# Performance work log

Measured on AMD Instinct MI355X. Metric: run time of the kernel, lower is better.

Reference implementation:

```python
import jax, jax.numpy as jnp
import numpy as np

BETA1, BETA2, BETA3 = 0.9, 0.8, 0.9
DECAY1, INC1 = 0.05, 5.0
DECAY3, INC3 = 0.05, 5.0
LATENCY = 4.0
B_CONST = 0.15
LIF1_MIN, LIF1_MAX = 150.0, 400.0
LIF3_MIN, LIF3_MAX = 50.0, 200.0
A_P, A_M, TAU_P, TAU_M = 0.01, 0.01, 20.0, 20.0  # exponential STDP params (params1/2/3)


def stdp(dt):
    # exponential STDP curve: potentiate when post fires after pre (dt>=0), depress otherwise
    return jnp.where(dt >= 0, A_P * jnp.exp(-dt / TAU_P), -A_M * jnp.exp(dt / TAU_M))


def setup_inputs() -> dict:
    key = jax.random.key(0)
    k1, k2, k3, k4 = jax.random.split(key, 4)
    H, N, C = 8192, 4096, 128
    return {
        "image": jax.random.uniform(k1, (N,), jnp.float32),
        "W1": jax.random.uniform(k2, (H, N), jnp.float32),
        "W2": jax.random.uniform(k3, (N, H), jnp.float32),
        "W3": jax.random.uniform(k4, (C, N), jnp.float32),
        "thr1": 100.0 * jnp.ones((H,), jnp.float32),
        "thr2": 5.0 * jnp.ones((N,), jnp.float32),
        "thr3": 100.0 * jnp.ones((C,), jnp.float32),
        "time": 256,
        "pw": 8,
    }


def reference(image, W1, W2, W3, thr1, thr2, thr3, time, pw):
    N = image.shape[0]
    H = W1.shape[0]
    C = W3.shape[0]
    T = int(time)
    Tf = jnp.float32(T)

    img_t = Tf * image  # input spike times, [N]
    # rate -> pulse encoding: input_spikes[t, i] = 1 for t in [floor(img_t[i]), floor(img_t[i])+pw)
    t_axis = jnp.arange(T, dtype=jnp.float32)[:, None]          # [T,1]
    start = jnp.floor(img_t)[None, :]                            # [1,N]
    input_spikes = ((t_axis >= start) & (t_axis < start + pw)).astype(jnp.float32)  # [T,N]

    def wta(mem, th):
        # winner-take-all (snntorch inhibition=True): only argmax neuron may spike
        j = jnp.argmax(mem)
        fire = (mem[j] > th[j]).astype(mem.dtype)
        return fire * jax.nn.one_hot(j, mem.shape[0], dtype=mem.dtype)

    def step(carry, xs):
        mem1, mem2, mem3, th1, th3, r1, r2, r3, hid_act, out_act = carry
        x, t = xs
        # layer 1: Leaky LIF, inhibition, reset-to-zero
        mem1 = BETA1 * mem1 + jnp.dot(W1, x)
        spk1 = wta(mem1, th1)
        mem1 = mem1 * (1.0 - spk1)
        # layer 2: Leaky LIF, no inhibition, reset-by-subtract
        mem2 = BETA2 * mem2 + jnp.dot(W2, spk1)
        spk2 = (mem2 > thr2).astype(mem2.dtype)
        mem2 = mem2 - spk2 * thr2
        # layer 3 (clustering): Leaky LIF, inhibition, zeroed after any spike
        mem3 = BETA3 * mem3 + jnp.dot(W3, spk2)
        spk3 = wta(mem3, th3)
        mem3 = mem3 - spk3 * th3
        mem3 = jnp.where(jnp.sum(spk3) > 0, 0.0, mem3)
        # first-spike-time recon (recon stays at first nonzero spk*(t+1))
        r1 = jnp.where(r1 != 0, r1, spk1 * (t + 1.0))
        r2 = jnp.where(r2 != 0, r2, spk2 * (t + 1.0))
        r3 = jnp.where(r3 != 0, r3, spk3 * (t + 1.0))
        hid_act = hid_act + spk1
        out_act = out_act + spk2
        # adaptive thresholds: homeostatic decay + spike-triggered increase, clamped
        th1 = jnp.clip(th1 - DECAY1 + INC1 * spk1, LIF1_MIN, LIF1_MAX)
        th3 = jnp.clip(th3 - DECAY3 + INC3 * spk3, LIF3_MIN, LIF3_MAX)
        return (mem1, mem2, mem3, th1, th3, r1, r2, r3, hid_act, out_act), None

    z = jnp.zeros
    carry0 = (z(H), z(N), z(C), thr1, thr3, z(H), z(N), z(C), z(H), z(N))
    (mem1, mem2, mem3, th1, th3, r1, r2, r3, hid_act, out_act), _ = jax.lax.scan(
        step, carry0, (input_spikes, jnp.arange(T, dtype=jnp.float32)))

    # neurons that never spiked get time T
    r1 = jnp.where(r1 == 0, Tf, r1)
    r2 = jnp.where(r2 == 0, Tf, r2)
    r3 = jnp.where(r3 == 0, Tf, r3)

    # STDP weight updates (exponential), same structure as PresentImage
    hid_mask = (hid_act > 0).astype(jnp.float32)
    delta_t1 = (r1[:, None] - img_t[None, :]) * hid_mask[:, None]      # [H,N]
    W1_new = W1 + stdp(delta_t1)
    delta_t2 = r2[:, None] - r1[None, :]                                # [N,H]
    zeta = (Tf - r1) * hid_mask / Tf                                    # [H]
    rho = (r2 - LATENCY - img_t) / Tf + B_CONST                         # [N]
    W2_new = jnp.clip(W2 + stdp(delta_t2) * (rho[:, None] * zeta[None, :]), 0.0, 1.0)
    delta_t3 = r3[:, None] - r2[None, :]                                # [C,N]
    W3_new = W3 + stdp(delta_t3)

    error = (img_t - (r2 - LATENCY)) / Tf
    error_scalar = jnp.sum(jnp.square(error))
    return (error, error_scalar, r1, r2, r3, W1_new, W2_new, W3_new)
```

## Files before the change

kernel.cpp:

```cpp
#include <hip/hip_runtime.h>
#include <cstdint>
#include <cstddef>

#define Hn 8192
#define Nn 4096
#define Cn 128
#define Tt 256
#define CAP 192
#define CHUNK 8
#define RING 16

typedef unsigned long long ull;

__device__ __forceinline__ float th_lazy2(float b, float lo, float hi, int nup){
    if (nup <= 0) return b;
    float a = fminf(fmaxf(__fsub_rn(b, 0.05f), lo), hi);
    if (nup == 1) return a;
    return fmaxf(__fsub_rn(a, __fmul_rn(0.05f, (float)(nup - 1))), lo);
}

__device__ __forceinline__ float clamp01(float v){
    return fminf(fmaxf(v, 0.f), 1.f);
}

template<int CTRL>
__device__ __forceinline__ int dpp_i(int x, int old){
    return __builtin_amdgcn_update_dpp(old, x, CTRL, 0xf, 0xf, false);
}
__device__ __forceinline__ float wave_max_f(float v){
    const int NEG = __float_as_int(-3.4e38f);
#define STEPM(C) { float o = __int_as_float(dpp_i<C>(__float_as_int(v), NEG)); v = fmaxf(v, o); }
    STEPM(0x111) STEPM(0x112) STEPM(0x114) STEPM(0x118) STEPM(0x142) STEPM(0x143)
#undef STEPM
    return __int_as_float(__builtin_amdgcn_readlane(__float_as_int(v), 63));
}
__device__ __forceinline__ int wave_argmax_l(float bv, int bh, float &wv, int &wh){
    float v = wave_max_f(bv);
    ull tie = __ballot(bv == v);
    int tl = __ffsll((long long)tie) - 1;
    int h = __builtin_amdgcn_readlane(bh, tl);
    if (__builtin_expect(__popcll(tie) > 1, 0)){
        ull m = tie & (tie - 1);
        while (m){
            int l2 = __ffsll((long long)m) - 1;
            int h2 = __builtin_amdgcn_readlane(bh, l2);
            if (h2 < h){ h = h2; tl = l2; }
            m &= m - 1;
        }
    }
    wv = v; wh = h; return tl;
}
__device__ __forceinline__ float rl_f(float x, int l){
    return __int_as_float(__builtin_amdgcn_readlane(__float_as_int(x), l));
}

__global__ __launch_bounds__(1024) void k_prep(const float* __restrict__ image,
        int* __restrict__ boff, int* __restrict__ sidx, unsigned* __restrict__ anyv,
        float* __restrict__ imgt, float* __restrict__ eiP, float* __restrict__ eiM){
    __shared__ int s_start[Nn];
    __shared__ int s_c4[4][Tt];
    __shared__ int s_boff[Tt + 1];
    int tid = threadIdx.x;
    for (int i = tid; i < Nn; i += 1024){
        float im = image[i];
        float img = __fmul_rn(256.f, im);
        s_start[i] = (int)floorf(img);
        imgt[i] = img;
        eiP[i] = __expf(img * 0.05f);
        eiM[i] = __expf(-img * 0.05f);
    }
    if (tid < Tt) anyv[tid] = 0u;
    __syncthreads();
    int b = tid & 255, q = tid >> 8;
    {
        int c = 0;
        for (int k = 0; k < 1024; ++k) c += (s_start[q * 1024 + k] == b) ? 1 : 0;
        s_c4[q][b] = c;
    }
    __syncthreads();
    if (tid == 0){
        int acc = 0;
        for (int bb = 0; bb < Tt; ++bb){
            s_boff[bb] = acc;
            acc += s_c4[0][bb] + s_c4[1][bb] + s_c4[2][bb] + s_c4[3][bb];
        }
        s_boff[Tt] = acc;
    }
    __syncthreads();
    if (tid <= Tt) boff[tid] = s_boff[tid];
    int p = s_boff[b];
    if (q > 0) p += s_c4[0][b];
    if (q > 1) p += s_c4[1][b];
    if (q > 2) p += s_c4[2][b];
    for (int k = 0; k < 1024; ++k){
        int i = q * 1024 + k;
        if (s_start[i] == b) sidx[p++] = i;
    }
}

__global__ __launch_bounds__(256) void k_gbuckets(const float* __restrict__ W1,
        const int* __restrict__ boff, const int* __restrict__ sidx,
        float* __restrict__ G_T, float* __restrict__ o_W1){
    __shared__ float rows[2][Nn];
    int tid = threadIdx.x;
    int h0 = blockIdx.x * 2;
    for (int r = 0; r < 2; ++r){
        const float4* src = (const float4*)(W1 + (size_t)(h0 + r) * Nn);
        float4* dst = (float4*)rows[r];
        for (int j = tid; j < Nn / 4; j += 256) dst[j] = src[j];
    }
    __syncthreads();
    int t = tid;
    int b0 = boff[t], b1 = boff[t + 1];
    float s0 = 0.f, s1 = 0.f;
    for (int k = b0; k < b1; ++k){
        int i = sidx[k];
        s0 += rows[0][i]; s1 += rows[1][i];
    }
    G_T[(size_t)(h0 + 0) * Tt + t] = s0;
    G_T[(size_t)(h0 + 1) * Tt + t] = s1;
    for (int r = 0; r < 2; ++r){
        const float4* srw = (const float4*)rows[r];
        float4* dw = (float4*)(o_W1 + (size_t)(h0 + r) * Nn);
        for (int j = tid; j < Nn / 4; j += 256){
            float4 s = srw[j];
            s.x = __fadd_rn(s.x, 0.01f); s.y = __fadd_rn(s.y, 0.01f);
            s.z = __fadd_rn(s.z, 0.01f); s.w = __fadd_rn(s.w, 0.01f);
            dw[j] = s;
        }
    }
}

__global__ __launch_bounds__(256) void k_c1M(const float* __restrict__ G_T,
        float* __restrict__ M, float* __restrict__ r1pre, float* __restrict__ o_r1){
    __shared__ float tile[32][Tt + 1];
    __shared__ float c1s[32][Tt + 1];
    const int tid = threadIdx.x;
    const int h0 = blockIdx.x * 32;
    for (int r = 0; r < 32; ++r) tile[r][tid] = G_T[(size_t)(h0 + r) * Tt + tid];
    __syncthreads();
    {
        int hs = tid & 31, ts = tid >> 5;
        for (int tb = 0; tb < 32; ++tb){
            int t = tb * 8 + ts;
            int lo = (t - 7 < 0) ? 0 : t - 7;
            float s = 0.f;
            for (int u = lo; u <= t; ++u) s += tile[hs][u];
            c1s[hs][t] = s;
        }
    }
    __syncthreads();
    if (tid < 32){
        float m = 0.f;
        for (int t = 0; t < Tt; ++t){
            m = __fadd_rn(__fmul_rn(0.9f, m), c1s[tid][t]);
            M[(size_t)t * Hn + h0 + tid] = m;
        }
        r1pre[h0 + tid] = 0.f;
        o_r1[h0 + tid] = 256.f;
    }
}

__global__ __launch_bounds__(256) void k_sel(const float* __restrict__ M,
        float2* __restrict__ cand2, float* __restrict__ gvcap){
    const int t = blockIdx.x, tid = threadIdx.x;
    __shared__ float s_row[Hn];
    __shared__ unsigned s_hist[256];
    __shared__ unsigned s_suf[256];
    __shared__ unsigned s_pref;
    __shared__ int s_rank;
    __shared__ int s_cnt;
    __shared__ int s_idx[CAP + 64];
    {
        const float4* src = (const float4*)(M + (size_t)t * Hn);
        float4* d4 = (float4*)s_row;
        for (int j = tid; j < Hn / 4; j += 256) d4[j] = src[j];
    }
    if (tid == 0){ s_pref = 0u; s_rank = CAP; s_cnt = 0; }
    __syncthreads();
#pragma unroll
    for (int b = 3; b >= 0; --b){
        s_hist[tid] = 0u;
        __syncthreads();
        unsigned pref = s_pref;
        int r = s_rank;
        for (int k = 0; k < 32; ++k){
            unsigned u = __float_as_uint(s_row[tid + (k << 8)]);
            bool match = (b == 3) ? true : ((u >> ((b + 1) * 8)) == pref);
            if (match) atomicAdd(&s_hist[(u >> (b * 8)) & 255], 1u);
        }
        __syncthreads();
        s_suf[tid] = s_hist[tid];
        __syncthreads();
#pragma unroll
        for (int off = 1; off < 256; off <<= 1){
            unsigned v = (tid + off < 256) ? s_suf[tid + off] : 0u;
            __syncthreads();
            s_suf[tid] += v;
            __syncthreads();
        }
        unsigned above = s_suf[tid] - s_hist[tid];
        if ((int)above < r && r <= (int)s_suf[tid]){
            s_pref = (pref << 8) | (unsigned)tid;
            s_rank = r - (int)above;
        }
        __syncthreads();
    }
    unsigned V = s_pref;
    for (int k = 0; k < 32; ++k){
        int i = tid + (k << 8);
        unsigned u = __float_as_uint(s_row[i]);
        if (u >= V){
            int p = atomicAdd(&s_cnt, 1);
            if (p < CAP + 64) s_idx[p] = i;
        }
    }
    __syncthreads();
    int c = s_cnt;
    bool ovf = (c > CAP);
    if (tid == 0) gvcap[t] = ovf ? 3.4e38f : __uint_as_float(V);
    for (int i = tid; i < CAP; i += 256){
        float2 e;
        if (!ovf && i < c){
            int ix = s_idx[i];
            e = make_float2(s_row[ix], __int_as_float(ix | (1 << 15)));
        } else {
            e = make_float2(-1.f, 0.f);
        }
        cand2[(size_t)t * CAP + i] = e;
    }
}

#define NB_W2 1024
#define NB_W3T 128

union FusedLDS {
    struct {
        float4 mst[Hn];
        float2 ring[RING][CAP];
        float  vcr[RING];
        int j1[Tt];
        unsigned bm[256];
    } w;
    float tl[64][65];
};

__global__ __launch_bounds__(1024, 1) void k_fused(
        const float* __restrict__ M, const float2* __restrict__ cand2,
        const float* __restrict__ gvcap, const float* __restrict__ thr1,
        const float* __restrict__ W2, const float* __restrict__ W3,
        float* __restrict__ o_W2, float* __restrict__ W3T,
        float* __restrict__ r1pre, float* __restrict__ o_r1,
        int* __restrict__ j1s, int* __restrict__ mh, int* __restrict__ nRout){
    __shared__ FusedLDS u;
    const int bid = blockIdx.x;
    const int tid = threadIdx.x;

    if (bid >= 1 && bid < 1 + NB_W2){
        size_t base = (size_t)(bid - 1) * 8192;
        const float4* src = (const float4*)W2;
        float4* dst = (float4*)o_W2;
        for (int i = tid; i < 8192; i += 4096){
            float4 a0 = src[base + i];
            float4 a1 = src[base + i + 1024];
            float4 a2 = src[base + i + 2048];
            float4 a3 = src[base + i + 3072];
            a0.x = clamp01(a0.x); a0.y = clamp01(a0.y); a0.z = clamp01(a0.z); a0.w = clamp01(a0.w);
            a1.x = clamp01(a1.x); a1.y = clamp01(a1.y); a1.z = clamp01(a1.z); a1.w = clamp01(a1.w);
            a2.x = clamp01(a2.x); a2.y = clamp01(a2.y); a2.z = clamp01(a2.z); a2.w = clamp01(a2.w);
            a3.x = clamp01(a3.x); a3.y = clamp01(a3.y); a3.z = clamp01(a3.z); a3.w = clamp01(a3.w);
            dst[base + i]        = a0;
            dst[base + i + 1024] = a1;
            dst[base + i + 2048] = a2;
            dst[base + i + 3072] = a3;
        }
        return;
    }
    if (bid >= 1 + NB_W2){
        int r = bid - 1 - NB_W2;
        int bx = r & 63, by = r >> 6;
        int n0 = bx * 64, c0 = by * 64;
        for (int e = tid; e < 64 * 64; e += 1024){
            int rr = e >> 6, cc = e & 63;
            u.tl[rr][cc] = W3[(size_t)(c0 + rr) * Nn + n0 + cc];
        }
        __syncthreads();
        for (int e = tid; e < 64 * 64; e += 1024){
            int rn = e >> 6, cc = e & 63;
            W3T[(size_t)(n0 + rn) * Cn + c0 + cc] = u.tl[cc][rn];
        }
        return;
    }

    for (int h = tid; h < Hn; h += 1024)
        u.w.mst[h] = make_float4(0.f, -1.f, thr1[h], 0.f);
    for (int e = tid; e < CHUNK * CAP; e += 1024){
        int so = e / CAP, j = e - so * CAP;
        u.w.ring[so][j] = cand2[(size_t)so * CAP + j];
    }
    if (tid < CHUNK) u.w.vcr[tid] = gvcap[tid];
    __syncthreads();

    const int lane = tid & 63;
    const float Lc = -0.15200309344504997f;

    for (int c = 0; c < Tt / CHUNK; ++c){
        if (tid >= 64 && c + 1 < Tt / CHUNK){
            for (int e = tid - 64; e < CHUNK * CAP; e += 960){
                int so = e / CAP, j = e - so * CAP;
                int step = (c + 1) * CHUNK + so;
                u.w.ring[step & (RING - 1)][j] = cand2[(size_t)step * CAP + j];
            }
            if (tid - 64 < CHUNK){
                int step = (c + 1) * CHUNK + (tid - 64);
                u.w.vcr[step & (RING - 1)] = gvcap[step];
            }
        }
        if (tid < 64){
            for (int s = 0; s < CHUNK; ++s){
                const int t = c * CHUNK + s;
                const int slot = t & (RING - 1);
                const float tf = (float)t;
                float2 e0 = u.w.ring[slot][lane];
                float2 e1 = u.w.ring[slot][64 + lane];
                float2 e2 = u.w.ring[slot][128 + lane];
                float vc = u.w.vcr[slot];
                int m0b = __float_as_int(e0.y), m1b = __float_as_int(e1.y), m2b = __float_as_int(e2.y);
                int h0 = m0b & 8191, h1 = m1b & 8191, h2 = m2b & 8191;
                float4 g0 = u.w.mst[h0];
                float4 g1 = u.w.mst[h1];
                float4 g2 = u.w.mst[h2];
                float bm = -3.4e38f; int bhh = 0x7FFFFFFF;
                float braw = 0.f, bts = 0.f, bthb = 0.f;
#define CPROC(ee, mb, hh, gg) { \
                float dd = __fsub_rn(tf, gg.y); \
                float mem = __fsub_rn(ee.x, __fmul_rn(exp2f(__fmul_rn(dd, Lc)), gg.x)); \
                if (!((mb >> 15) & 1)) mem = -3.4e38f; \
                if (mem > bm || (mem == bm && hh < bhh)){ bm = mem; bhh = hh; braw = ee.x; bts = gg.y; bthb = gg.z; } }
                CPROC(e0, m0b, h0, g0) CPROC(e1, m1b, h1, g1) CPROC(e2, m2b, h2, g2)
#undef CPROC
                float wv; int wh;
                int wl = wave_argmax_l(bm, bhh, wv, wh);
                float raw = rl_f(braw, wl), tsv = rl_f(bts, wl), thb = rl_f(bthb, wl);
                int skip = 0;
                if (__builtin_expect(wv < vc, 0)){
                    if (t > 0 && vc < 150.f){
                        skip = 1;
                    } else {
                        float fv = -3.4e38f; int fh = 0x7FFFFFFF;
                        float fraw = 0.f, fts = 0.f, fthb = 0.f;
                        const float4* Mrow4 = (const float4*)(M + (size_t)t * Hn);
                        for (int q = 0; q < 32; ++q){
                            int e = q * 64 + lane;
                            float4 mv = Mrow4[e];
                            int ib = e * 4;
                            float4 q0 = u.w.mst[ib+0], q1 = u.w.mst[ib+1], q2 = u.w.mst[ib+2], q3 = u.w.mst[ib+3];
#define FPROC(comp, gg, o2) { float x = mv.comp; float dd = __fsub_rn(tf, gg.y); \
                            float mm = __fsub_rn(x, __fmul_rn(exp2f(__fmul_rn(dd, Lc)), gg.x)); \
                            int hh2 = ib + o2; \
                            if (mm > fv || (mm == fv && hh2 < fh)){ fv = mm; fh = hh2; fraw = x; fts = gg.y; fthb = gg.z; } }
                            FPROC(x, q0, 0) FPROC(y, q1, 1) FPROC(z, q2, 2) FPROC(w, q3, 3)
#undef FPROC
                        }
                        wl = wave_argmax_l(fv, fh, wv, wh);
                        raw = rl_f(fraw, wl); tsv = rl_f(fts, wl); fthb = rl_f(fthb, wl); thb = fthb;
                    }
                }
                int fire = 0; float thnew = 0.f;
                if (!skip){
                    float te = th_lazy2(thb, 150.f, 400.f, t - (int)tsv - 1);
                    if (wv > te){
                        fire = 1;
                        thnew = fminf(fmaxf(__fadd_rn(__fsub_rn(te, 0.05f), 5.0f), 150.f), 400.f);
                    }
                }
                if (fire){
                    if (lane == 0){
                        u.w.j1[t] = wh;
                        if (tsv < 0.f){ o_r1[wh] = tf + 1.f; r1pre[wh] = tf + 1.f; }
                        u.w.mst[wh] = make_float4(raw, tf, thnew, 0.f);
                    }
                } else {
                    if (lane == 0) u.w.j1[t] = -1;
                }
            }
        }
        __syncthreads();
    }
    if (tid >= 64) return;

    for (int i = lane; i < 256; i += 64) u.w.bm[i] = 0u;
    asm volatile("s_waitcnt lgkmcnt(0)" ::: "memory");
    for (int i = lane; i < Tt; i += 64){
        int h = u.w.j1[i];
        j1s[i] = h;
        if (h >= 0) atomicOr(&u.w.bm[h >> 5], 1u << (h & 31));
    }
    asm volatile("s_waitcnt lgkmcnt(0)" ::: "memory");
    unsigned w0 = u.w.bm[lane*4+0], w1 = u.w.bm[lane*4+1];
    unsigned w2 = u.w.bm[lane*4+2], w3 = u.w.bm[lane*4+3];
    int c = __popc(w0) + __popc(w1) + __popc(w2) + __popc(w3);
    int inc = c;
#pragma unroll
    for (int off = 1; off < 64; off <<= 1){
        int v = __shfl_up(inc, off);
        if (lane >= off) inc += v;
    }
    int b = inc - c;
#define WALK(wrd, k) { unsigned ww = wrd; while (ww){ int bt = __ffs(ww) - 1; ww &= ww - 1; \
        mh[b++] = ((lane * 4 + k) << 5) | bt; } }
    WALK(w0, 0) WALK(w1, 1) WALK(w2, 2) WALK(w3, 3)
#undef WALK
    if (lane == 63) *nRout = inc;
}

__global__ __launch_bounds__(64) void k_lif2(const float* __restrict__ W2,
        const int* __restrict__ j1s, const float* __restrict__ thr2,
        float* __restrict__ o_r2, ull* __restrict__ spkb, unsigned* __restrict__ anyv){
    __shared__ int s_j[Tt];
    int lane = threadIdx.x, blk = blockIdx.x;
    for (int i = lane; i < Tt; i += 64) s_j[i] = j1s[i];
    __syncthreads();
    int n = blk * 64 + lane;
    const float* Wrow = W2 + (size_t)n * Hn;
    float tv = thr2[n], m = 0.f, rp = 0.f;
#define LD(dst, tt) { int hh = s_j[tt]; dst = (hh >= 0) ? Wrow[hh] : 0.f; }
#define STEP(uu, tt) { m = __fadd_rn(__fmul_rn(0.8f, m), uu); int f = 0; \
        if (m > tv){ m = __fsub_rn(m, tv); if (rp == 0.f) rp = (float)((tt) + 1); f = 1; } \
        ull mask = __ballot(f); \
        if (lane == 0){ spkb[(tt) * 64 + blk] = mask; if (mask) atomicOr(&anyv[tt], 1u); } }
    float u0, u1, u2, u3;
    LD(u0, 0) LD(u1, 1) LD(u2, 2) LD(u3, 3)
    for (int g = 0; g < 64; ++g){
        float v0 = 0.f, v1 = 0.f, v2 = 0.f, v3 = 0.f;
        if (g < 63){
            int bb = (g + 1) * 4;
            LD(v0, bb) LD(v1, bb + 1) LD(v2, bb + 2) LD(v3, bb + 3)
        }
        int t = g * 4;
        STEP(u0, t) STEP(u1, t + 1) STEP(u2, t + 2) STEP(u3, t + 3)
        u0 = v0; u1 = v1; u2 = v2; u3 = v3;
    }
#undef LD
#undef STEP
    o_r2[n] = (rp == 0.f) ? 256.f : rp;
}

__global__ __launch_bounds__(128, 1) void k_sim3(const ull* __restrict__ spkb,
        const unsigned* __restrict__ anyv, const float* __restrict__ W3T,
        const float* __restrict__ thr3, float* __restrict__ o_r3){
    int tid = threadIdx.x, lane = tid & 63, w = tid >> 6;
    __shared__ ull s_spk[Tt * 64];
    __shared__ unsigned s_any[Tt];
    __shared__ ull s_r2[2];
    __shared__ int s_fire;
    {
        const uint4* src = (const uint4*)spkb;
        uint4* dst = (uint4*)s_spk;
        for (int i = tid; i < Tt * 64 / 2; i += 128) dst[i] = src[i];
    }
    for (int i = tid; i < Tt; i += 128) s_any[i] = anyv[i];
    float m = 0.f, th0 = thr3[tid], rp = 0.f, thv = 0.f;
    int ts = -1, zero = 1;
    __syncthreads();
    for (int t = 0; t < Tt; ++t){
        if (zero && s_any[t] == 0u) continue;
        float d = 0.f;
        if (s_any[t]){
            for (int ww = 0; ww < 64; ++ww){
                ull bits = s_spk[t * 64 + ww];
                while (bits){
                    int b2 = __ffsll((long long)bits) - 1;
                    bits &= bits - 1;
                    d = __fadd_rn(d, W3T[(size_t)(ww * 64 + b2) * Cn + tid]);
                }
            }
        }
        m = __fadd_rn(__fmul_rn(0.9f, m), d);
        ull k = (((ull)__float_as_uint(m >= 0.f ? m : 0.f)) << 32) | (unsigned)(8191 - tid);
        if (!(m >= 0.f)) k = (unsigned)(8191 - tid);
#pragma unroll
        for (int off = 32; off >= 1; off >>= 1){
            ull o = __shfl_down(k, off);
            if (o > k) k = o;
        }
        if (lane == 0) s_r2[w] = k;
        __syncthreads();
        ull wk = s_r2[0] > s_r2[1] ? s_r2[0] : s_r2[1];
        int wc = 8191 - (int)(wk & 0xFFFFu);
        float wv = __uint_as_float((unsigned)(wk >> 32));
        if (tid == wc){
            float te = (ts < 0) ? th_lazy2(th0, 50.f, 200.f, t)
                                : th_lazy2(thv, 50.f, 200.f, t - ts - 1);
            int f = (wv > te) ? 1 : 0;
            s_fire = f;
            if (f){
                thv = fminf(fmaxf(__fadd_rn(__fsub_rn(te, 0.05f), 5.0f), 50.f), 200.f);
                ts = t;
                if (rp == 0.f) rp = (float)(t + 1);
            }
        }
        __syncthreads();
        if (s_fire){ m = 0.f; zero = 1; }
        else zero = 0;
        __syncthreads();
    }
    o_r3[tid] = (rp == 0.f) ? 256.f : rp;
}

__global__ __launch_bounds__(256) void k_post(const float* __restrict__ image,
        const float* __restrict__ r1pre, const float* __restrict__ o_r1,
        const float* __restrict__ o_r2, const float* __restrict__ o_r3,
        const float* __restrict__ imgt, const float* __restrict__ eiP,
        const float* __restrict__ eiM,
        const float* __restrict__ W1, const float* __restrict__ W3,
        const int* __restrict__ mh, const int* __restrict__ nRout,
        float* __restrict__ zeta, float* __restrict__ rho,
        float* __restrict__ Pv, float* __restrict__ Qv,
        float* __restrict__ o_err, float* __restrict__ o_es,
        float* __restrict__ o_W1, float* __restrict__ o_W3){
    const int bid = blockIdx.x;
    const int tid = threadIdx.x;
    if (bid == 0){
        for (int h = tid; h < Hn; h += 256){
            float r1f = o_r1[h];
            float mask = (r1pre[h] != 0.f) ? 1.f : 0.f;
            float z = __fmul_rn(__fmul_rn(__fsub_rn(256.f, r1f), mask), 0.00390625f);
            zeta[h] = z;
            Pv[h] = __expf(r1f * 0.05f) * z;
            Qv[h] = __expf(-r1f * 0.05f) * z;
        }
        float acc = 0.f;
        for (int n = tid; n < Nn; n += 256){
            float img = __fmul_rn(256.f, image[n]);
            float r2f = o_r2[n];
            float e = __fmul_rn(__fsub_rn(img, __fsub_rn(r2f, 4.0f)), 0.00390625f);
            o_err[n] = e;
            rho[n] = __fadd_rn(__fmul_rn(__fsub_rn(__fsub_rn(r2f, 4.0f), img), 0.00390625f), 0.15f);
            acc = __fadd_rn(acc, __fmul_rn(e, e));
        }
        __shared__ float red[4];
        for (int off = 32; off >= 1; off >>= 1) acc += __shfl_down(acc, off);
        int lane = tid & 63, w = tid >> 6;
        if (lane == 0) red[w] = acc;
        __syncthreads();
        if (tid == 0) *o_es = red[0] + red[1] + red[2] + red[3];
        return;
    }
    if (bid <= 256){
        int slot = bid - 1;
        if (slot >= *nRout) return;
        int h = mh[slot];
        float r1f = o_r1[h];
        float a = 0.01f * __expf(-r1f * 0.05f);
        float b = 0.01f * __expf( r1f * 0.05f);
        const float4* src = (const float4*)(W1 + (size_t)h * Nn);
        float4* dst = (float4*)(o_W1 + (size_t)h * Nn);
        const float4* ig = (const float4*)imgt;
        const float4* p4 = (const float4*)eiP;
        const float4* m4 = (const float4*)eiM;
        for (int i = tid; i < Nn / 4; i += 256){
            float4 s = src[i];
            float4 im = ig[i], pp = p4[i], mm = m4[i];
            s.x += (r1f >= im.x) ? a * pp.x : -(b * mm.x);
            s.y += (r1f >= im.y) ? a * pp.y : -(b * mm.y);
            s.z += (r1f >= im.z) ? a * pp.z : -(b * mm.z);
            s.w += (r1f >= im.w) ? a * pp.w : -(b * mm.w);
            dst[i] = s;
        }
        return;
    }
    {
        int cc = bid - 257;
        float r3f = o_r3[cc];
        float a = 0.01f * __expf(-r3f * 0.05f);
        float b = 0.01f * __expf( r3f * 0.05f);
        const float4* src = (const float4*)(W3 + (size_t)cc * Nn);
        float4* dst = (float4*)(o_W3 + (size_t)cc * Nn);
        const float4* r24 = (const float4*)o_r2;
        for (int i = tid; i < Nn / 4; i += 256){
            float4 s = src[i]; float4 rv = r24[i];
            s.x += (r3f >= rv.x) ? a * __expf(rv.x * 0.05f) : -(b * __expf(-rv.x * 0.05f));
            s.y += (r3f >= rv.y) ? a * __expf(rv.y * 0.05f) : -(b * __expf(-rv.y * 0.05f));
            s.z += (r3f >= rv.z) ? a * __expf(rv.z * 0.05f) : -(b * __expf(-rv.z * 0.05f));
            s.w += (r3f >= rv.w) ? a * __expf(rv.w * 0.05f) : -(b * __expf(-rv.w * 0.05f));
            dst[i] = s;
        }
    }
}

__global__ __launch_bounds__(128) void k_w2fix(
        const float* __restrict__ o_r1, const float* __restrict__ Pv,
        const float* __restrict__ Qv, const float* __restrict__ o_r2,
        const float* __restrict__ rho, const int* __restrict__ mh,
        const int* __restrict__ nRout, float* __restrict__ o_W2){
    __shared__ int   s_h[Tt];
    __shared__ float s_rv[Tt], s_pp[Tt], s_qq[Tt];
    int n = blockIdx.x, tid = threadIdx.x;
    int nRv = *nRout;
    for (int s = tid; s < nRv; s += 128){
        int h = mh[s];
        s_h[s] = h; s_rv[s] = o_r1[h]; s_pp[s] = Pv[h]; s_qq[s] = Qv[h];
    }
    __syncthreads();
    float r2f = o_r2[n], rh = rho[n];
    float A = 0.01f * rh * __expf(-r2f * 0.05f);
    float B = 0.01f * rh * __expf( r2f * 0.05f);
    for (int s = tid; s < nRv; s += 128){
        size_t idx = (size_t)n * Hn + s_h[s];
        float w = o_W2[idx];
        float rv = s_rv[s];
        w = clamp01(w + ((r2f >= rv) ? A * s_pp[s] : -(B * s_qq[s])));
        o_W2[idx] = w;
    }
}

extern "C" void kernel_launch(void* const* d_in, const int* in_sizes, int n_in,
                              void* d_out, int out_size, void* d_ws, size_t ws_size,
                              hipStream_t stream){
    const float* image = (const float*)d_in[0];
    const float* W1   = (const float*)d_in[1];
    const float* W2   = (const float*)d_in[2];
    const float* W3   = (const float*)d_in[3];
    const float* thr1 = (const float*)d_in[4];
    const float* thr2 = (const float*)d_in[5];
    const float* thr3 = (const float*)d_in[6];

    float* out  = (float*)d_out;
    float* o_err = out;
    float* o_es  = out + 4096;
    float* o_r1  = out + 4097;
    float* o_r2  = out + 12289;
    float* o_r3  = out + 16385;
    float* o_W1  = out + 16513;
    float* o_W2  = o_W1 + (size_t)Hn * Nn;
    float* o_W3  = o_W2 + (size_t)Nn * Hn;

    float* ws = (float*)d_ws;
    float* G_T   = ws;
    float* M     = G_T + (size_t)Hn * Tt;
    float* W3T   = M + (size_t)Tt * Hn;
    float2* cand2 = (float2*)(W3T + (size_t)Nn * Cn);
    float* gvcap = (float*)(cand2 + (size_t)Tt * CAP);
    ull* spkb    = (ull*)(gvcap + Tt);
    float* r1pre = (float*)(spkb + (size_t)Tt * 64);
    float* zeta  = r1pre + Hn;
    float* rho   = zeta + Hn;
    float* imgt  = rho + Nn;
    float* eiP   = imgt + Nn;
    float* eiM   = eiP + Nn;
    float* Pv    = eiM + Nn;
    float* Qv    = Pv + Hn;
    int* boff   = (int*)(Qv + Hn);
    int* sidx   = boff + (Tt + 1);
    int* j1s    = sidx + Nn;
    int* mh     = j1s + Tt;
    int* nRout  = mh + 256;
    unsigned* anyv = (unsigned*)(nRout + 1);

    k_prep<<<1, 1024, 0, stream>>>(image, boff, sidx, anyv, imgt, eiP, eiM);
    k_gbuckets<<<Hn / 2, 256, 0, stream>>>(W1, boff, sidx, G_T, o_W1);
    k_c1M<<<Hn / 32, 256, 0, stream>>>(G_T, M, r1pre, o_r1);
    k_sel<<<Tt, 256, 0, stream>>>(M, cand2, gvcap);
    k_fused<<<1 + NB_W2 + NB_W3T, 1024, 0, stream>>>(
        M, cand2, gvcap, thr1, W2, W3, o_W2, W3T, r1pre, o_r1, j1s, mh, nRout);
    k_lif2<<<Nn / 64, 64, 0, stream>>>(W2, j1s, thr2, o_r2, spkb, anyv);
    k_sim3<<<1, 128, 0, stream>>>(spkb, anyv, W3T, thr3, o_r3);
    k_post<<<1 + 256 + 128, 256, 0, stream>>>(image, r1pre, o_r1, o_r2, o_r3,
        imgt, eiP, eiM, W1, W3, mh, nRout, zeta, rho, Pv, Qv, o_err, o_es, o_W1, o_W3);
    k_w2fix<<<Nn, 128, 0, stream>>>(o_r1, Pv, Qv, o_r2, rho, mh, nRout, o_W2);
}
```

Baseline: 504.0 us.

## Replace dense per-neuron LDS state with slot-indexed table of fired neurons

The fused serial-scan block previously kept a 128 KB float4 state array for all 8192 hidden neurons in LDS, filling it with thr1 at startup. It now keeps a 16-bit slot index per neuron plus a small table of states for neurons that have actually fired. Candidates carry their thr1 value, written by the selection kernel, so initialising the state only needs to zero the slot array. This cuts LDS footprint and setup work, at the cost of one extra dependent LDS lookup per candidate and wider float4 candidate records in global memory and the ring buffer.

```diff
diff --git a/kernel.cpp b/kernel.cpp
--- a/kernel.cpp
+++ b/kernel.cpp
@@ -162,7 +162,8 @@
 }
 
 __global__ __launch_bounds__(256) void k_sel(const float* __restrict__ M,
-        float2* __restrict__ cand2, float* __restrict__ gvcap){
+        const float* __restrict__ thr1, float4* __restrict__ cand,
+        float* __restrict__ gvcap){
     const int t = blockIdx.x, tid = threadIdx.x;
     __shared__ float s_row[Hn];
     __shared__ unsigned s_hist[256];
@@ -220,14 +221,14 @@
     bool ovf = (c > CAP);
     if (tid == 0) gvcap[t] = ovf ? 3.4e38f : __uint_as_float(V);
     for (int i = tid; i < CAP; i += 256){
-        float2 e;
+        float4 e;
         if (!ovf && i < c){
             int ix = s_idx[i];
-            e = make_float2(s_row[ix], __int_as_float(ix | (1 << 15)));
+            e = make_float4(s_row[ix], __int_as_float(ix | (1 << 15)), thr1[ix], 0.f);
         } else {
-            e = make_float2(-1.f, 0.f);
-        }
-        cand2[(size_t)t * CAP + i] = e;
+            e = make_float4(-1.f, 0.f, 0.f, 0.f);
+        }
+        cand[(size_t)t * CAP + i] = e;
     }
 }
 
@@ -236,8 +237,9 @@
 
 union FusedLDS {
     struct {
-        float4 mst[Hn];
-        float2 ring[RING][CAP];
+        float4 ring[RING][CAP];
+        float4 fst[260];
+        unsigned short slot[Hn];
         float  vcr[RING];
         int j1[Tt];
         unsigned bm[256];
@@ -246,7 +248,7 @@
 };
 
 __global__ __launch_bounds__(1024, 1) void k_fused(
-        const float* __restrict__ M, const float2* __restrict__ cand2,
+        const float* __restrict__ M, const float4* __restrict__ cand,
         const float* __restrict__ gvcap, const float* __restrict__ thr1,
         const float* __restrict__ W2, const float* __restrict__ W3,
         float* __restrict__ o_W2, float* __restrict__ W3T,
@@ -292,24 +294,29 @@
         return;
     }
 
-    for (int h = tid; h < Hn; h += 1024)
-        u.w.mst[h] = make_float4(0.f, -1.f, thr1[h], 0.f);
+    {
+        uint4 z = make_uint4(0u, 0u, 0u, 0u);
+        uint4* p = (uint4*)u.w.slot;
+        for (int i = tid; i < Hn * 2 / 16; i += 1024) p[i] = z;
+    }
+    if (tid == 0) u.w.fst[0] = make_float4(0.f, -1.f, 0.f, 0.f);
     for (int e = tid; e < CHUNK * CAP; e += 1024){
         int so = e / CAP, j = e - so * CAP;
-        u.w.ring[so][j] = cand2[(size_t)so * CAP + j];
+        u.w.ring[so][j] = cand[(size_t)so * CAP + j];
     }
     if (tid < CHUNK) u.w.vcr[tid] = gvcap[tid];
     __syncthreads();
 
     const int lane = tid & 63;
     const float Lc = -0.15200309344504997f;
+    int nR = 1;
 
     for (int c = 0; c < Tt / CHUNK; ++c){
         if (tid >= 64 && c + 1 < Tt / CHUNK){
             for (int e = tid - 64; e < CHUNK * CAP; e += 960){
                 int so = e / CAP, j = e - so * CAP;
                 int step = (c + 1) * CHUNK + so;
-                u.w.ring[step & (RING - 1)][j] = cand2[(size_t)step * CAP + j];
+                u.w.ring[step & (RING - 1)][j] = cand[(size_t)step * CAP + j];
             }
             if (tid - 64 < CHUNK){
                 int step = (c + 1) * CHUNK + (tid - 64);
@@ -321,23 +328,25 @@
                 const int t = c * CHUNK + s;
                 const int slot = t & (RING - 1);
                 const float tf = (float)t;
-                float2 e0 = u.w.ring[slot][lane];
-                float2 e1 = u.w.ring[slot][64 + lane];
-                float2 e2 = u.w.ring[slot][128 + lane];
+                float4 e0 = u.w.ring[slot][lane];
+                float4 e1 = u.w.ring[slot][64 + lane];
+                float4 e2 = u.w.ring[slot][128 + lane];
                 float vc = u.w.vcr[slot];
                 int m0b = __float_as_int(e0.y), m1b = __float_as_int(e1.y), m2b = __float_as_int(e2.y);
                 int h0 = m0b & 8191, h1 = m1b & 8191, h2 = m2b & 8191;
-                float4 g0 = u.w.mst[h0];
-                float4 g1 = u.w.mst[h1];
-                float4 g2 = u.w.mst[h2];
+                int sl0 = u.w.slot[h0], sl1 = u.w.slot[h1], sl2 = u.w.slot[h2];
+                float4 g0 = u.w.fst[sl0];
+                float4 g1 = u.w.fst[sl1];
+                float4 g2 = u.w.fst[sl2];
                 float bm = -3.4e38f; int bhh = 0x7FFFFFFF;
                 float braw = 0.f, bts = 0.f, bthb = 0.f;
-#define CPROC(ee, mb, hh, gg) { \
+#define CPROC(ee, mb, hh, gg, sl) { \
                 float dd = __fsub_rn(tf, gg.y); \
                 float mem = __fsub_rn(ee.x, __fmul_rn(exp2f(__fmul_rn(dd, Lc)), gg.x)); \
+                float tb = (sl == 0) ? ee.z : gg.z; \
                 if (!((mb >> 15) & 1)) mem = -3.4e38f; \
-                if (mem > bm || (mem == bm && hh < bhh)){ bm = mem; bhh = hh; braw = ee.x; bts = gg.y; bthb = gg.z; } }
-                CPROC(e0, m0b, h0, g0) CPROC(e1, m1b, h1, g1) CPROC(e2, m2b, h2, g2)
+                if (mem > bm || (mem == bm && hh < bhh)){ bm = mem; bhh = hh; braw = ee.x; bts = gg.y; bthb = tb; } }
+                CPROC(e0, m0b, h0, g0, sl0) CPROC(e1, m1b, h1, g1, sl1) CPROC(e2, m2b, h2, g2, sl2)
 #undef CPROC
                 float wv; int wh;
                 int wl = wave_argmax_l(bm, bhh, wv, wh);
@@ -354,12 +363,16 @@
                             int e = q * 64 + lane;
                             float4 mv = Mrow4[e];
                             int ib = e * 4;
-                            float4 q0 = u.w.mst[ib+0], q1 = u.w.mst[ib+1], q2 = u.w.mst[ib+2], q3 = u.w.mst[ib+3];
-#define FPROC(comp, gg, o2) { float x = mv.comp; float dd = __fsub_rn(tf, gg.y); \
+                            int q0s = u.w.slot[ib+0], q1s = u.w.slot[ib+1];
+                            int q2s = u.w.slot[ib+2], q3s = u.w.slot[ib+3];
+                            float4 q0 = u.w.fst[q0s], q1 = u.w.fst[q1s];
+                            float4 q2 = u.w.fst[q2s], q3 = u.w.fst[q3s];
+#define FPROC(comp, gg, ss, o2) { float x = mv.comp; float dd = __fsub_rn(tf, gg.y); \
                             float mm = __fsub_rn(x, __fmul_rn(exp2f(__fmul_rn(dd, Lc)), gg.x)); \
                             int hh2 = ib + o2; \
-                            if (mm > fv || (mm == fv && hh2 < fh)){ fv = mm; fh = hh2; fraw = x; fts = gg.y; fthb = gg.z; } }
-                            FPROC(x, q0, 0) FPROC(y, q1, 1) FPROC(z, q2, 2) FPROC(w, q3, 3)
+                            float tb2 = (ss == 0) ? thr1[hh2] : gg.z; \
+                            if (mm > fv || (mm == fv && hh2 < fh)){ fv = mm; fh = hh2; fraw = x; fts = gg.y; fthb = tb2; } }
+                            FPROC(x, q0, q0s, 0) FPROC(y, q1, q1s, 1) FPROC(z, q2, q2s, 2) FPROC(w, q3, q3s, 3)
 #undef FPROC
                         }
                         wl = wave_argmax_l(fv, fh, wv, wh);
@@ -378,8 +391,10 @@
                     if (lane == 0){
                         u.w.j1[t] = wh;
                         if (tsv < 0.f){ o_r1[wh] = tf + 1.f; r1pre[wh] = tf + 1.f; }
-                        u.w.mst[wh] = make_float4(raw, tf, thnew, 0.f);
+                        u.w.fst[nR] = make_float4(raw, tf, thnew, 0.f);
+                        u.w.slot[wh] = (unsigned short)nR;
                     }
+                    nR++;
                 } else {
                     if (lane == 0) u.w.j1[t] = -1;
                 }
@@ -640,8 +655,8 @@
     float* G_T   = ws;
     float* M     = G_T + (size_t)Hn * Tt;
     float* W3T   = M + (size_t)Tt * Hn;
-    float2* cand2 = (float2*)(W3T + (size_t)Nn * Cn);
-    float* gvcap = (float*)(cand2 + (size_t)Tt * CAP);
+    float4* cand = (float4*)(W3T + (size_t)Nn * Cn);
+    float* gvcap = (float*)(cand + (size_t)Tt * CAP);
     ull* spkb    = (ull*)(gvcap + Tt);
     float* r1pre = (float*)(spkb + (size_t)Tt * 64);
     float* zeta  = r1pre + Hn;
@@ -661,9 +676,9 @@
     k_prep<<<1, 1024, 0, stream>>>(image, boff, sidx, anyv, imgt, eiP, eiM);
     k_gbuckets<<<Hn / 2, 256, 0, stream>>>(W1, boff, sidx, G_T, o_W1);
     k_c1M<<<Hn / 32, 256, 0, stream>>>(G_T, M, r1pre, o_r1);
-    k_sel<<<Tt, 256, 0, stream>>>(M, cand2, gvcap);
+    k_sel<<<Tt, 256, 0, stream>>>(M, thr1, cand, gvcap);
     k_fused<<<1 + NB_W2 + NB_W3T, 1024, 0, stream>>>(
-        M, cand2, gvcap, thr1, W2, W3, o_W2, W3T, r1pre, o_r1, j1s, mh, nRout);
+        M, cand, gvcap, thr1, W2, W3, o_W2, W3T, r1pre, o_r1, j1s, mh, nRout);
     k_lif2<<<Nn / 64, 64, 0, stream>>>(W2, j1s, thr2, o_r2, spkb, anyv);
     k_sim3<<<1, 128, 0, stream>>>(spkb, anyv, W3T, thr3, o_r3);
     k_post<<<1 + 256 + 128, 256, 0, stream>>>(image, r1pre, o_r1, o_r2, o_r3,
```

Measured after the change: 556.4 us. 10.4% more time.
